# Kernel optimization log

Measured on AMD Instinct MI355X. Metric: run time of the kernel, lower is better.

## Reference

```python
import math
import jax, jax.numpy as jnp
import numpy as np

B, H, N, D = 1, 16, 4096, 64
SINK_SIZE = 32
NUM_PROJS = 7
BLOCK_SIZE = 256
SAMPLE_SIZE = 256
MIN_SEQ_LEN = 1024
_SAMPLE_KEY = jax.random.key(1234)

def _hamming_perm(num_projs):
    a = np.array([0, 1])
    for _ in range(num_projs - 1):
        a = np.concatenate([a, a[::-1] + a.shape[0]])
    return jnp.asarray(a, dtype=jnp.int32)

_PERM = _hamming_perm(NUM_PROJS)
_MASK = jnp.asarray(2 ** np.arange(NUM_PROJS), dtype=jnp.int32)

def lsh_hash(x, proj_dir):
    # x: [b,h,n,d], proj_dir: [d,r] -> Gray-code-permuted bucket ids [b,h,n]
    rotated = jnp.einsum('bhnd,dr->bhnr', x, proj_dir)
    bin_ids = jnp.sum((rotated > 0).astype(jnp.int32) * _MASK, axis=-1)
    return _PERM[bin_ids]

def indexing(x, idx, chunk_size=-1):
    # gather rows along axis 2, optionally zero-pad to a multiple of chunk_size
    out = jnp.take_along_axis(x, idx[..., None], axis=2)
    if chunk_size > 0 and out.shape[2] % chunk_size != 0:
        pad = (-out.shape[2]) % chunk_size
        out = jnp.pad(out, ((0, 0), (0, 0), (0, pad), (0, 0)))
    return out

def exact_attention(q, k, v, scale, causal=False, bias=None):
    qk = jnp.einsum('bhqd,bhkd->bhqk', q, k) * scale
    if causal:
        nq, nk = q.shape[2], k.shape[2]
        cmask = jnp.triu(jnp.full((nq, nk), jnp.finfo(q.dtype).min, dtype=q.dtype), k=1)
        qk = qk + cmask
    if bias is not None:
        qk = qk + bias
    lse = jax.nn.logsumexp(qk, axis=-1, keepdims=True)
    attn = jnp.einsum('bhqk,bhkd->bhqd', jnp.exp(qk - lse), v)
    return attn, lse

def add_self_attentions(attn1, lse1, attn2, lse2):
    # attn = (attn1*e^lse1 + attn2*e^lse2)/(e^lse1+e^lse2); lse = log(e^lse1+e^lse2)
    c = jax.nn.sigmoid(lse1 - lse2)
    attn = c * attn1 + (1 - c) * attn2
    lse = jnp.logaddexp(lse1, lse2)
    return attn, lse

def forward_no_causal_mask(q, k, v, scale, proj_dir, ctr):
    b, h, nq, d = q.shape
    nk = k.shape[2]
    if MIN_SEQ_LEN > nq:
        return exact_attention(q, k, v, scale, causal=False)
    # 1) sortLSH block-diagonal attention
    q_sort_idx = jnp.argsort(lsh_hash(q, proj_dir), axis=2)  # stable
    k_sort_idx = jnp.argsort(lsh_hash(k, proj_dir), axis=2)
    q_sort_idx_inv = jnp.argsort(q_sort_idx, axis=2)
    q_sorted = indexing(q, q_sort_idx, BLOCK_SIZE)
    k_sorted = indexing(k, k_sort_idx, BLOCK_SIZE)
    v_sorted = indexing(v, k_sort_idx, BLOCK_SIZE)
    num_blocks = k_sorted.shape[2] // BLOCK_SIZE
    q_block = q_sorted.shape[2] // num_blocks
    qs = q_sorted.reshape(-1, 1, q_block, d)
    ks = k_sorted.reshape(-1, 1, BLOCK_SIZE, d)
    vs = v_sorted.reshape(-1, 1, BLOCK_SIZE, d)
    attn_block, lse_block = exact_attention(qs, ks, vs, scale, causal=False)
    attn_block = attn_block.reshape(b, h, q_sorted.shape[2], d)[:, :, :nq, :]
    lse_block = lse_block.reshape(b, h, q_sorted.shape[2], 1)[:, :, :nq, :]
    q_sorted = q_sorted[:, :, :nq, :]
    k_sorted = k_sorted[:, :, :nk, :]
    v_sorted = v_sorted[:, :, :nk, :]
    # 2) residual via uniform sampling (block-diag entries masked out)
    if SAMPLE_SIZE > 0 and nq > q_block and nk > BLOCK_SIZE:
        skey = jax.random.fold_in(_SAMPLE_KEY, ctr[0]); ctr[0] += 1
        sampled = jax.random.randint(skey, (b, h, SAMPLE_SIZE), 0, nk)
        v_sub = indexing(v_sorted, sampled)
        k_sub = indexing(k_sorted, sampled)
        q_blk_id = jnp.arange(nq) // q_block                 # [nq]
        k_blk_id = sampled // BLOCK_SIZE                     # [b,h,s]
        bias = (q_blk_id[None, None, :, None] == k_blk_id[:, :, None, :]).astype(q.dtype) * jnp.finfo(q.dtype).min
        attn_res, lse_res = exact_attention(q_sorted, k_sub, v_sub, scale, causal=False, bias=bias)
        lse_res = lse_res + math.log(nk / SAMPLE_SIZE)
        attn, lse = add_self_attentions(attn_block, lse_block, attn_res, lse_res)
    else:
        attn, lse = attn_block, lse_block
    # restore original row order
    attn = indexing(attn, q_sort_idx_inv)
    lse = indexing(lse, q_sort_idx_inv)
    return attn, lse

def hyper_causal(q, k, v, scale, proj_dir, ctr):
    b, h, n, d = q.shape
    if n <= MIN_SEQ_LEN:
        return exact_attention(q, k, v, scale, causal=True)
    n_orig = n
    if n % 2:
        q = jnp.pad(q, ((0, 0), (0, 0), (0, 1), (0, 0)))
        k = jnp.pad(k, ((0, 0), (0, 0), (0, 1), (0, 0)))
        v = jnp.pad(v, ((0, 0), (0, 0), (0, 1), (0, 0)))
    half = q.shape[2] // 2
    # recurse on the two diagonal halves (folded into head dim)
    attn_bd, lse_bd = hyper_causal(q.reshape(b, 2 * h, half, d), k.reshape(b, 2 * h, half, d), v.reshape(b, 2 * h, half, d), scale, proj_dir, ctr)
    attn_bd = attn_bd.reshape(b, h, -1, d)
    lse_bd = lse_bd.reshape(b, h, -1, 1)
    # off-diagonal lower-left block, unmasked
    attn_un, lse_un = forward_no_causal_mask(q[:, :, half:, :], k[:, :, :half, :], v[:, :, :half, :], scale, proj_dir, ctr)
    attn_up, lse_up = attn_bd[:, :, :half, :], lse_bd[:, :, :half, :]
    attn_dn, lse_dn = add_self_attentions(attn_bd[:, :, half:, :], lse_bd[:, :, half:, :], attn_un, lse_un)
    attn = jnp.concatenate([attn_up, attn_dn], axis=2)
    lse = jnp.concatenate([lse_up, lse_dn], axis=2)
    if n_orig % 2:
        attn = attn[:, :, :-1, :]
        lse = lse[:, :, :-1, :]
    return attn, lse

def _forward(query, key, value, proj_dir):
    b, h, n, d = query.shape
    scale = d ** (-0.5)
    sink = min(SINK_SIZE, n)
    prefix_attn, prefix_lse = exact_attention(query, key[:, :, :sink, :], value[:, :, :sink, :], scale, causal=True)
    if sink >= n:
        return prefix_attn
    ctr = [0]
    tail_attn, tail_lse = hyper_causal(query[:, :, sink:, :], key[:, :, sink:, :], value[:, :, sink:, :], scale, proj_dir, ctr)
    padded_tail_attn = jnp.zeros_like(prefix_attn).at[:, :, sink:, :].set(tail_attn)
    neg_inf = jnp.full_like(prefix_lse[:, :, :sink, :], jnp.finfo(prefix_lse.dtype).min)
    padded_tail_lse = jnp.concatenate([neg_inf, tail_lse], axis=2)
    attn, _ = add_self_attentions(prefix_attn, prefix_lse, padded_tail_attn, padded_tail_lse)
    return attn

def setup_inputs() -> dict:
    rng = jax.random.key(0)
    k1, k2, k3, k4 = jax.random.split(rng, 4)
    return {
        'query': jax.random.normal(k1, (B, H, N, D), jnp.float32),
        'key': jax.random.normal(k2, (B, H, N, D), jnp.float32),
        'value': jax.random.normal(k3, (B, H, N, D), jnp.float32),
        'proj_dir': jax.random.normal(k4, (D, NUM_PROJS), jnp.float32),
    }

def reference(query, key, value, proj_dir):
    return _forward(query, key, value, proj_dir)
```

## Files before the change

kernel.cpp:

```cpp
#include <hip/hip_runtime.h>
#include <hip/hip_bf16.h>
#include <math.h>
#include <stdint.h>

#define H_ 16
#define N_ 4096
#define NT_ 4064
#define NL_ 2032
#define SINK_ 32
#define SAMP_ 256
#define SCALE_ 0.125f
#define QSCALE_ 0.18033688f
#define M0L2_ 11.5415606f
#define M0_ 8.0f
#define NEGBIG_ -3.0e38f
#define LOGOFF_L2_ 2.9886841f

typedef unsigned int uint;
typedef unsigned short ushort;
typedef short bf16x8 __attribute__((ext_vector_type(8)));
typedef float f32x4 __attribute__((ext_vector_type(4)));

union B8 { uint4 u; bf16x8 b; };

__device__ __forceinline__ f32x4 mfma16(const B8& a, const B8& b, f32x4 c) {
  return __builtin_amdgcn_mfma_f32_16x16x32_bf16(a.b, b.b, c, 0, 0, 0);
}

__device__ __forceinline__ uint bfpack(float a, float b) {
  uint ua = __float_as_uint(a), ub = __float_as_uint(b);
  ua += 0x7fffu + ((ua >> 16) & 1u);
  ub += 0x7fffu + ((ub >> 16) & 1u);
  return (ua >> 16) | (ub & 0xffff0000u);
}

__device__ __forceinline__ uint cvtpk(float a, float b) {
  union { __hip_bfloat162 h; uint u; } r;
  r.h.x = __float2bfloat16(a);
  r.h.y = __float2bfloat16(b);
  return r.u;
}

__device__ __forceinline__ float logaddexpf_(float a, float b) {
  float mx = fmaxf(a, b);
  return mx + __logf(__expf(a - mx) + __expf(b - mx));
}

__device__ __forceinline__ uint32_t rotl32_(uint32_t v, uint32_t d) {
  return (v << d) | (v >> (32u - d));
}

__device__ inline void tf2x32(uint32_t k0, uint32_t k1, uint32_t& x0, uint32_t& x1) {
  uint32_t ks2 = k0 ^ k1 ^ 0x1BD11BDAu;
  x0 += k0; x1 += k1;
#define TFR(r) { x0 += x1; x1 = rotl32_(x1, r); x1 ^= x0; }
  TFR(13u) TFR(15u) TFR(26u) TFR(6u)
  x0 += k1;  x1 += ks2 + 1u;
  TFR(17u) TFR(29u) TFR(16u) TFR(24u)
  x0 += ks2; x1 += k0 + 2u;
  TFR(13u) TFR(15u) TFR(26u) TFR(6u)
  x0 += k0;  x1 += k1 + 3u;
  TFR(17u) TFR(29u) TFR(16u) TFR(24u)
  x0 += k1;  x1 += ks2 + 4u;
  TFR(13u) TFR(15u) TFR(26u) TFR(6u)
  x0 += ks2; x1 += k0 + 5u;
#undef TFR
}

__device__ __forceinline__ void nomax_sm(f32x4 s[4], float& ssum) {
#pragma unroll
  for (int st = 0; st < 4; ++st)
#pragma unroll
    for (int r = 0; r < 4; ++r) {
      s[st][r] = __builtin_exp2f(s[st][r]);
      ssum += s[st][r];
    }
}

__device__ __forceinline__ void pv144(const f32x4 s[4], f32x4 o[4],
                                      const char* vbase, char* pw, int g) {
#pragma unroll
  for (int hk2 = 0; hk2 < 2; ++hk2) {
    const f32x4 pa = s[2 * hk2], pc = s[2 * hk2 + 1];
    *(uint2*)(pw + 8 * g)      = make_uint2(cvtpk(pa[0], pa[1]), cvtpk(pa[2], pa[3]));
    *(uint2*)(pw + 32 + 8 * g) = make_uint2(cvtpk(pc[0], pc[1]), cvtpk(pc[2], pc[3]));
    B8 pf, vf;
    pf.u = *(const uint4*)(pw + g * 16);
    vf.u = *(const uint4*)(vbase + 0 * 2304 + hk2 * 64); o[0] = mfma16(vf, pf, o[0]);
    vf.u = *(const uint4*)(vbase + 1 * 2304 + hk2 * 64); o[1] = mfma16(vf, pf, o[1]);
    vf.u = *(const uint4*)(vbase + 2 * 2304 + hk2 * 64); o[2] = mfma16(vf, pf, o[2]);
    vf.u = *(const uint4*)(vbase + 3 * 2304 + hk2 * 64); o[3] = mfma16(vf, pf, o[3]);
  }
}

__global__ __launch_bounds__(256) void kern_packhash(
    const float* __restrict__ K, const float* __restrict__ V, const float* __restrict__ Q,
    const float* __restrict__ proj,
    ushort* __restrict__ Kb, ushort* __restrict__ Vb, ushort* __restrict__ Vt,
    int* __restrict__ hq, int* __restrict__ hk) {
  const int bb = blockIdx.x;
  const int tid = threadIdx.x;
  if (bb < 2048) {
    const size_t idx = (size_t)bb * 256 + tid;
    const float4* s = (const float4*)(K + idx * 8);
    float4 f0 = s[0], f1 = s[1];
    uint4 p = make_uint4(bfpack(f0.x, f0.y), bfpack(f0.z, f0.w),
                         bfpack(f1.x, f1.y), bfpack(f1.z, f1.w));
    *(uint4*)(Kb + idx * 8) = p;
    return;
  }
  if (bb < 3072) {
    __shared__ ushort tr[64 * 72];
    const int u = bb - 2048;
    const int h = u >> 6, nt = u & 63;
    const int n0 = nt * 64;
    const size_t hN = (size_t)h * N_;
    const int nloc = tid >> 2, dpart = (tid & 3) * 16;
    const float4* src = (const float4*)(V + (hN + n0 + nloc) * 64 + dpart);
    float4 f0 = src[0], f1 = src[1], f2 = src[2], f3 = src[3];
    uint p0 = bfpack(f0.x, f0.y), p1 = bfpack(f0.z, f0.w);
    uint p2 = bfpack(f1.x, f1.y), p3 = bfpack(f1.z, f1.w);
    uint p4 = bfpack(f2.x, f2.y), p5 = bfpack(f2.z, f2.w);
    uint p6 = bfpack(f3.x, f3.y), p7 = bfpack(f3.z, f3.w);
    ushort* vbdst = Vb + (hN + n0 + nloc) * 64 + dpart;
    ((uint4*)vbdst)[0] = make_uint4(p0, p1, p2, p3);
    ((uint4*)vbdst)[1] = make_uint4(p4, p5, p6, p7);
    uint pv[8] = {p0, p1, p2, p3, p4, p5, p6, p7};
#pragma unroll
    for (int j = 0; j < 8; ++j) {
      tr[(dpart + 2 * j    ) * 72 + nloc] = (ushort)(pv[j] & 0xffffu);
      tr[(dpart + 2 * j + 1) * 72 + nloc] = (ushort)(pv[j] >> 16);
    }
    __syncthreads();
    const int d = tid >> 2, np = (tid & 3) * 16;
    const uint4* tp = (const uint4*)(tr + d * 72 + np);
    uint4 t0 = tp[0], t1 = tp[1];
    ushort* dst = Vt + ((size_t)(h * 64 + d)) * 4096 + n0 + np;
    ((uint4*)dst)[0] = t0;
    ((uint4*)dst)[1] = t1;
    return;
  }
  __shared__ float pr[448];
  const int u = bb - 3072;
  const int h = u & 15, tile = (u >> 4) & 7, which = u >> 7;
  for (int t = tid; t < 448; t += 256) pr[t] = proj[t];
  __syncthreads();
  const int i = tile * 256 + tid;
  if (i >= NL_) return;
  const int orig = (which == 0) ? (SINK_ + NL_ + i) : (SINK_ + i);
  const float4* x = (const float4*)((which == 0 ? Q : K) + ((size_t)h * N_ + orig) * 64);
  float xr[64];
#pragma unroll
  for (int d = 0; d < 16; ++d) {
    float4 g = x[d];
    xr[4*d+0] = g.x; xr[4*d+1] = g.y; xr[4*d+2] = g.z; xr[4*d+3] = g.w;
  }
  int bin = 0;
#pragma unroll
  for (int r = 0; r < 7; ++r) {
    float acc = 0.f;
#pragma unroll
    for (int d = 0; d < 64; ++d) acc = fmaf(xr[d], pr[d * 7 + r], acc);
    if (acc > 0.f) bin |= (1 << r);
  }
  const int g = bin ^ (bin >> 1);
  (which == 0 ? hq : hk)[h * NL_ + i] = g;
}

__global__ __launch_bounds__(256) void kern_sortsamp(
    const int* __restrict__ hq, const int* __restrict__ hk,
    int* __restrict__ q_sort, int* __restrict__ k_sort,
    int* __restrict__ samp_pos, int* __restrict__ samp_orig) {
  const int h = blockIdx.x, which = blockIdx.y;
  const int tid = threadIdx.x;

  __shared__ unsigned char keys8[NL_];
  __shared__ ushort M[64 * 130];
  __shared__ int btot[128];
  __shared__ int bscan[128];
  __shared__ ushort srt[NL_];

  const int* src = (which == 0 ? hq : hk) + h * NL_;
  for (int u = tid; u < 64 * 130 / 2; u += 256) ((uint*)M)[u] = 0u;
  for (int u = tid; u < NL_; u += 256) keys8[u] = (unsigned char)src[u];
  __syncthreads();

  if (tid < 64) {
    const int c = tid;
#pragma unroll 4
    for (int j = 0; j < 32; ++j) {
      const int u = c * 32 + j;
      if (u < NL_) ++M[c * 130 + keys8[u]];
    }
  }
  __syncthreads();

  if (tid < 128) {
    const int b = tid;
    int run = 0;
    for (int c = 0; c < 64; ++c) {
      const int v = M[c * 130 + b];
      M[c * 130 + b] = (ushort)run;
      run += v;
    }
    btot[b] = run;
    bscan[b] = run;
  }
  __syncthreads();

  for (int ofs = 1; ofs < 128; ofs <<= 1) {
    int v = 0;
    if (tid < 128 && tid >= ofs) v = bscan[tid - ofs];
    __syncthreads();
    if (tid < 128) bscan[tid] += v;
    __syncthreads();
  }

  int* dst = (which == 0 ? q_sort : k_sort) + h * NL_;
  if (tid < 64) {
    const int c = tid;
    for (int j = 0; j < 32; ++j) {
      const int u = c * 32 + j;
      if (u < NL_) {
        const int k = keys8[u];
        const int pos = (bscan[k] - btot[k]) + M[c * 130 + k];
        M[c * 130 + k] += 1;
        dst[pos] = u;
        srt[pos] = (ushort)u;
      }
    }
  }
  __syncthreads();

  if (which == 1) {
    const int s = tid;
    uint32_t a0 = 0u, a1 = 0u; tf2x32(0u, 1234u, a0, a1);
    uint32_t b0 = 0u, b1 = 0u; tf2x32(a0, a1, b0, b1);
    uint32_t c0 = 0u, c1 = 1u; tf2x32(a0, a1, c0, c1);
    const uint32_t j = (uint32_t)(h * SAMP_ + s);
    uint32_t h0 = 0u, h1 = j; tf2x32(b0, b1, h0, h1);
    uint32_t l0 = 0u, l1 = j; tf2x32(c0, c1, l0, l1);
    const uint32_t Hb = h0 ^ h1, Lb = l0 ^ l1;
    const uint32_t off = ((Hb % 2032u) * 16u + (Lb % 2032u)) % 2032u;
    samp_pos[h * SAMP_ + s] = (int)off;
    samp_orig[h * SAMP_ + s] = (int)srt[off];
  }
}

__global__ __launch_bounds__(256) void kern_attn_mfma(
    const float* __restrict__ Q, const ushort* __restrict__ Kb, const ushort* __restrict__ Vt,
    float* __restrict__ tail_attn, float* __restrict__ tail_lse,
    float* __restrict__ attn2, float* __restrict__ lse2) {
  __shared__ uint kk[4608];
  __shared__ uint vv[4352];
  __shared__ uint pbuf[1280];

  const int b = blockIdx.x;
  const int tid = threadIdx.x;
  const int lane = tid & 63, w = tid >> 6;
  const int g = lane >> 4, q = lane & 15;
  const uint4 z4 = make_uint4(0, 0, 0, 0);
  const f32x4 accb = {-M0L2_, -M0L2_, -M0L2_, -M0L2_};

  int h, q0, qbase, kbase, ntiles, p2vh = 0, chunkc = 0;
  bool causal;
  if (b < 256) {
    const int vh = b & 31; const int qt = b >> 5;
    h = vh >> 1; const int pp = vh & 1;
    q0 = qt * 128;
    qbase = SINK_ + pp * 2032 + 1016;
    kbase = SINK_ + pp * 2032;
    ntiles = 8; causal = false; p2vh = vh;
  } else {
    const int u = b - 256; const int vh = u & 63;
    const int qt = 7 - (u >> 6);
    h = vh >> 2; chunkc = vh & 3;
    q0 = qt * 128;
    qbase = SINK_ + chunkc * 1016;
    kbase = qbase;
    ntiles = qt + 1; causal = true;
  }
  const size_t hN = (size_t)h * N_;
  const int qrowA = q0 + w * 16 + q;
  const int qrowB = qrowA + 64;
  const int qcA = min(qrowA, 1015), qcB = min(qrowB, 1015);
  const int qwA_lo = q0 + w * 16, qwmaxA = qwA_lo + 15;
  const int qwB_lo = qwA_lo + 64;

  B8 qbA0, qbA1, qbB0, qbB1;
  {
    const float4* qp = (const float4*)(Q + (hN + qbase + qcA) * 64);
    float4 a = qp[2*g], c = qp[2*g+1], d = qp[8+2*g], e = qp[8+2*g+1];
    qbA0.u = make_uint4(bfpack(a.x*QSCALE_, a.y*QSCALE_), bfpack(a.z*QSCALE_, a.w*QSCALE_),
                        bfpack(c.x*QSCALE_, c.y*QSCALE_), bfpack(c.z*QSCALE_, c.w*QSCALE_));
    qbA1.u = make_uint4(bfpack(d.x*QSCALE_, d.y*QSCALE_), bfpack(d.z*QSCALE_, d.w*QSCALE_),
                        bfpack(e.x*QSCALE_, e.y*QSCALE_), bfpack(e.z*QSCALE_, e.w*QSCALE_));
    const float4* qp2 = (const float4*)(Q + (hN + qbase + qcB) * 64);
    a = qp2[2*g]; c = qp2[2*g+1]; d = qp2[8+2*g]; e = qp2[8+2*g+1];
    qbB0.u = make_uint4(bfpack(a.x*QSCALE_, a.y*QSCALE_), bfpack(a.z*QSCALE_, a.w*QSCALE_),
                        bfpack(c.x*QSCALE_, c.y*QSCALE_), bfpack(c.z*QSCALE_, c.w*QSCALE_));
    qbB1.u = make_uint4(bfpack(d.x*QSCALE_, d.y*QSCALE_), bfpack(d.z*QSCALE_, d.w*QSCALE_),
                        bfpack(e.x*QSCALE_, e.y*QSCALE_), bfpack(e.z*QSCALE_, e.w*QSCALE_));
  }
  f32x4 oA[4] = {{0,0,0,0},{0,0,0,0},{0,0,0,0},{0,0,0,0}};
  f32x4 oB[4] = {{0,0,0,0},{0,0,0,0},{0,0,0,0},{0,0,0,0}};
  float ssA = 0.f, ssB = 0.f;

  const int krow_l = tid >> 1, kpart = tid & 1;
  const int vrow = tid >> 2, vc32 = tid & 3;
  char* kdst = (char*)kk + krow_l * 144 + kpart * 64;
  char* vdst = (char*)vv + vrow * 272 + vc32 * 64;
  const char* kq = (const char*)kk + q * 144 + g * 16;
  const char* vq = (const char*)vv + q * 272 + g * 16;
  char* pw = (char*)pbuf + w * 1280 + q * 80;
  const size_t vtbase = ((size_t)(h * 64 + vrow)) * 4096 + kbase + vc32 * 32;

  uint4 kp0, kp1, kp2, kp3, va, va2, vb_, vb2;

#define LOADK(T) { const int kr = (T) * 128 + krow_l; \
    if (kr < 1016) { const uint4* s = (const uint4*)(Kb + (hN + kbase + kr) * 64 + kpart * 32); \
      kp0 = s[0]; kp1 = s[1]; kp2 = s[2]; kp3 = s[3]; } \
    else { kp0 = z4; kp1 = z4; kp2 = z4; kp3 = z4; } }
#define LOADV(T) { const uint4* sv = (const uint4*)(Vt + vtbase + (size_t)(T) * 128); \
    va = sv[0]; va2 = sv[1]; vb_ = sv[2]; vb2 = sv[3]; }

  LOADK(0) LOADV(0)

  for (int t = 0; t < ntiles; ++t) {
    const int kt = t * 128;
    __syncthreads();
    *(uint4*)kdst = kp0; *(uint4*)(kdst + 16) = kp1;
    *(uint4*)(kdst + 32) = kp2; *(uint4*)(kdst + 48) = kp3;
    *(uint4*)vdst = va; *(uint4*)(vdst + 16) = va2;
    *(uint4*)(vdst + 32) = vb_; *(uint4*)(vdst + 48) = vb2;
    __syncthreads();
    if (t + 1 < ntiles) { LOADK(t + 1) LOADV(t + 1) }

#pragma unroll
    for (int u2 = 0; u2 < 2; ++u2) {
      const int hb = kt + u2 * 64;
      const bool dA = !(causal && hb > qwmaxA);
      f32x4 sA[4], sB[4];
#pragma unroll
      for (int st = 0; st < 4; ++st) {
        B8 ka, kb2;
        ka.u  = *(const uint4*)(kq + (u2 * 64 + st * 16) * 144);
        kb2.u = *(const uint4*)(kq + (u2 * 64 + st * 16) * 144 + 64);
        if (dA) {
          f32x4 acc = accb;
          acc = mfma16(ka, qbA0, acc); acc = mfma16(kb2, qbA1, acc);
          sA[st] = acc;
        }
        f32x4 acc2 = accb;
        acc2 = mfma16(ka, qbB0, acc2); acc2 = mfma16(kb2, qbB1, acc2);
        sB[st] = acc2;
      }

      if (causal) {
        const int kb0 = hb + 4 * g;
        if (dA && hb + 63 > qwA_lo) {
#pragma unroll
          for (int st = 0; st < 4; ++st)
#pragma unroll
            for (int r = 0; r < 4; ++r)
              if (kb0 + st * 16 + r > qrowA) sA[st][r] = NEGBIG_;
        }
        if (hb + 63 > qwB_lo) {
#pragma unroll
          for (int st = 0; st < 4; ++st)
#pragma unroll
            for (int r = 0; r < 4; ++r)
              if (kb0 + st * 16 + r > qrowB) sB[st][r] = NEGBIG_;
        }
      } else if (hb + 63 >= 1016) {
        const int kb0 = hb + 4 * g;
#pragma unroll
        for (int st = 0; st < 4; ++st)
#pragma unroll
          for (int r = 0; r < 4; ++r)
            if (kb0 + st * 16 + r >= 1016) { sA[st][r] = NEGBIG_; sB[st][r] = NEGBIG_; }
      }

#define PVX(SS, OO) { \
      _Pragma("unroll") \
      for (int hk2 = 0; hk2 < 2; ++hk2) { \
        const f32x4 pa = SS[2 * hk2], pc = SS[2 * hk2 + 1]; \
        *(uint2*)(pw + 8 * g)      = make_uint2(cvtpk(pa[0], pa[1]), cvtpk(pa[2], pa[3])); \
        *(uint2*)(pw + 32 + 8 * g) = make_uint2(cvtpk(pc[0], pc[1]), cvtpk(pc[2], pc[3])); \
        B8 pf, vf; \
        pf.u = *(const uint4*)(pw + g * 16); \
        const int vo = u2 * 128 + hk2 * 64; \
        vf.u = *(const uint4*)(vq + 0 * 4352 + vo); OO[0] = mfma16(vf, pf, OO[0]); \
        vf.u = *(const uint4*)(vq + 1 * 4352 + vo); OO[1] = mfma16(vf, pf, OO[1]); \
        vf.u = *(const uint4*)(vq + 2 * 4352 + vo); OO[2] = mfma16(vf, pf, OO[2]); \
        vf.u = *(const uint4*)(vq + 3 * 4352 + vo); OO[3] = mfma16(vf, pf, OO[3]); \
      } }

      if (dA) {
        nomax_sm(sA, ssA);
        PVX(sA, oA)
      }
      nomax_sm(sB, ssB);
      PVX(sB, oB)
#undef PVX
    }
  }
#undef LOADK
#undef LOADV

  ssA += __shfl_xor(ssA, 16); ssA += __shfl_xor(ssA, 32);
  ssB += __shfl_xor(ssB, 16); ssB += __shfl_xor(ssB, 32);
#pragma unroll
  for (int fr = 0; fr < 2; ++fr) {
    const int qrow = fr == 0 ? qrowA : qrowB;
    if (qrow >= 1016) continue;
    f32x4* o = fr == 0 ? oA : oB;
    const float ss = fr == 0 ? ssA : ssB;
    const float lse = M0_ + __logf(ss);
    const float inv = 1.f / ss;
    if (causal) {
      const int trow = chunkc * 1016 + qrow;
      float* tp = tail_attn + ((size_t)h * NT_ + trow) * 64;
      *(f32x4*)(tp +  0 + 4*g) = o[0] * inv;
      *(f32x4*)(tp + 16 + 4*g) = o[1] * inv;
      *(f32x4*)(tp + 32 + 4*g) = o[2] * inv;
      *(f32x4*)(tp + 48 + 4*g) = o[3] * inv;
      if (lane < 16) tail_lse[h * NT_ + trow] = lse;
    } else {
      float* tp = attn2 + ((size_t)p2vh * 1016 + qrow) * 64;
      *(f32x4*)(tp +  0 + 4*g) = o[0] * inv;
      *(f32x4*)(tp + 16 + 4*g) = o[1] * inv;
      *(f32x4*)(tp + 32 + 4*g) = o[2] * inv;
      *(f32x4*)(tp + 48 + 4*g) = o[3] * inv;
      if (lane < 16) lse2[p2vh * 1016 + qrow] = lse;
    }
  }
}

__global__ __launch_bounds__(256) void kern_lsh_mfma(
    const float* __restrict__ Q, const ushort* __restrict__ Kb, const ushort* __restrict__ Vb,
    const int* __restrict__ q_sort, const int* __restrict__ k_sort,
    const int* __restrict__ samp_pos, const int* __restrict__ samp_orig,
    float* __restrict__ attn3, float* __restrict__ lse3) {
  __shared__ uint kk[2304];
  __shared__ uint vv[2304];
  __shared__ uint pbuf[1280];
  __shared__ float bias_s[64];

  const int b = blockIdx.x;
  const int h = b >> 4, pt = b & 15;
  const int tid = threadIdx.x;
  const int lane = tid & 63, w = tid >> 6;
  const int g = lane >> 4, q = lane & 15;
  const int blkq = pt >> 1;
  const size_t hN = (size_t)h * N_;

  const int pA = pt * 128 + w * 16 + q;
  const int pB = pA + 64;
  const int qiA = q_sort[h * NL_ + min(pA, NL_ - 1)];
  const int qiB = q_sort[h * NL_ + min(pB, NL_ - 1)];

  const int skey = tid >> 2, kpart = tid & 3;
  const int kpi = tid & 31, vdb = (tid >> 5) * 8;
  int kidx[8], vi0[8], vi1[8];
#pragma unroll
  for (int t = 0; t < 8; ++t) {
    if (t < 4) {
      const int slot = blkq * 256 + t * 64 + skey;
      kidx[t] = (slot < NL_) ? k_sort[h * NL_ + slot] : -1;
      const int s0 = blkq * 256 + t * 64 + 2 * kpi;
      vi0[t] = (s0 < NL_) ? k_sort[h * NL_ + s0] : -1;
      vi1[t] = (s0 + 1 < NL_) ? k_sort[h * NL_ + s0 + 1] : -1;
    } else {
      kidx[t] = samp_orig[h * SAMP_ + (t - 4) * 64 + skey];
      const int si = (t - 4) * 64 + 2 * kpi;
      vi0[t] = samp_orig[h * SAMP_ + si];
      vi1[t] = samp_orig[h * SAMP_ + si + 1];
    }
  }
  float biasr[4];
  if (tid < 64) {
#pragma unroll
    for (int j = 0; j < 4; ++j)
      biasr[j] = ((samp_pos[h * SAMP_ + j * 64 + tid] >> 8) == blkq) ? NEGBIG_ : LOGOFF_L2_;
  }

  B8 qbA0, qbA1, qbB0, qbB1;
  {
    const float4* qp = (const float4*)(Q + (hN + SINK_ + NL_ + qiA) * 64);
    float4 a = qp[2*g], c = qp[2*g+1], d = qp[8+2*g], e = qp[8+2*g+1];
    qbA0.u = make_uint4(bfpack(a.x*QSCALE_, a.y*QSCALE_), bfpack(a.z*QSCALE_, a.w*QSCALE_),
                        bfpack(c.x*QSCALE_, c.y*QSCALE_), bfpack(c.z*QSCALE_, c.w*QSCALE_));
    qbA1.u = make_uint4(bfpack(d.x*QSCALE_, d.y*QSCALE_), bfpack(d.z*QSCALE_, d.w*QSCALE_),
                        bfpack(e.x*QSCALE_, e.y*QSCALE_), bfpack(e.z*QSCALE_, e.w*QSCALE_));
    const float4* qp2 = (const float4*)(Q + (hN + SINK_ + NL_ + qiB) * 64);
    a = qp2[2*g]; c = qp2[2*g+1]; d = qp2[8+2*g]; e = qp2[8+2*g+1];
    qbB0.u = make_uint4(bfpack(a.x*QSCALE_, a.y*QSCALE_), bfpack(a.z*QSCALE_, a.w*QSCALE_),
                        bfpack(c.x*QSCALE_, c.y*QSCALE_), bfpack(c.z*QSCALE_, c.w*QSCALE_));
    qbB1.u = make_uint4(bfpack(d.x*QSCALE_, d.y*QSCALE_), bfpack(d.z*QSCALE_, d.w*QSCALE_),
                        bfpack(e.x*QSCALE_, e.y*QSCALE_), bfpack(e.z*QSCALE_, e.w*QSCALE_));
  }
  f32x4 oA[4] = {{0,0,0,0},{0,0,0,0},{0,0,0,0},{0,0,0,0}};
  f32x4 oB[4] = {{0,0,0,0},{0,0,0,0},{0,0,0,0},{0,0,0,0}};
  float ssA = 0.f, ssB = 0.f;
  const f32x4 accb = {-M0L2_, -M0L2_, -M0L2_, -M0L2_};

  char* kdst = (char*)kk + skey * 144 + kpart * 32;
  char* vdst = (char*)vv + vdb * 144 + kpi * 4;
  const char* kq = (const char*)kk + q * 144 + g * 16;
  const char* vq = (const char*)vv + q * 144 + g * 16;
  char* pw = (char*)pbuf + w * 1280 + q * 80;

  const uint4 z4 = make_uint4(0, 0, 0, 0);
  uint4 kp0, kp1, va, vb_;

#define LLOADK(T) { const int kr = kidx[T]; \
    if (kr >= 0) { const uint4* s = (const uint4*)(Kb + (hN + SINK_ + kr) * 64 + kpart * 16); \
      kp0 = s[0]; kp1 = s[1]; } else { kp0 = z4; kp1 = z4; } }
#define LLOADV(T) { const int r0 = vi0[T], r1 = vi1[T]; \
    va  = (r0 >= 0) ? *(const uint4*)(Vb + (hN + SINK_ + r0) * 64 + vdb) : z4; \
    vb_ = (r1 >= 0) ? *(const uint4*)(Vb + (hN + SINK_ + r1) * 64 + vdb) : z4; }

  LLOADK(0) LLOADV(0)

  for (int t = 0; t < 8; ++t) {
    __syncthreads();
    *(uint4*)kdst = kp0; *(uint4*)(kdst + 16) = kp1;
#define VP(JW, AW, BW) { \
    *(uint*)(vdst + (2*(JW)) * 144) = (AW & 0xffffu) | (BW << 16); \
    *(uint*)(vdst + (2*(JW) + 1) * 144) = (AW >> 16) | (BW & 0xffff0000u); }
    VP(0, va.x, vb_.x) VP(1, va.y, vb_.y) VP(2, va.z, vb_.z) VP(3, va.w, vb_.w)
#undef VP
    if (t >= 4 && tid < 64) bias_s[tid] = biasr[t - 4];
    __syncthreads();
    if (t + 1 < 8) { LLOADK(t + 1) LLOADV(t + 1) }

    f32x4 sA[4], sB[4];
#pragma unroll
    for (int st = 0; st < 4; ++st) {
      B8 ka, kb2;
      ka.u  = *(const uint4*)(kq + (st * 16) * 144);
      kb2.u = *(const uint4*)(kq + (st * 16) * 144 + 64);
      f32x4 acc = accb;
      acc = mfma16(ka, qbA0, acc); acc = mfma16(kb2, qbA1, acc);
      sA[st] = acc;
      f32x4 acc2 = accb;
      acc2 = mfma16(ka, qbB0, acc2); acc2 = mfma16(kb2, qbB1, acc2);
      sB[st] = acc2;
    }
    if (t >= 4) {
      const f32x4* bp = (const f32x4*)bias_s;
#pragma unroll
      for (int st = 0; st < 4; ++st) {
        sA[st] = sA[st] + bp[st * 4 + g];
        sB[st] = sB[st] + bp[st * 4 + g];
      }
    }

    nomax_sm(sA, ssA);
    pv144(sA, oA, vq, pw, g);
    nomax_sm(sB, ssB);
    pv144(sB, oB, vq, pw, g);
  }
#undef LLOADK
#undef LLOADV

  ssA += __shfl_xor(ssA, 16); ssA += __shfl_xor(ssA, 32);
  ssB += __shfl_xor(ssB, 16); ssB += __shfl_xor(ssB, 32);
#pragma unroll
  for (int fr = 0; fr < 2; ++fr) {
    const int p = fr == 0 ? pA : pB;
    if (p >= NL_) continue;
    const int qi = fr == 0 ? qiA : qiB;
    f32x4* o = fr == 0 ? oA : oB;
    const float ss = fr == 0 ? ssA : ssB;
    const float un = M0_ + __logf(ss);
    const float inv = 1.f / ss;
    float* tp = attn3 + ((size_t)h * NL_ + qi) * 64;
    *(f32x4*)(tp +  0 + 4*g) = o[0] * inv;
    *(f32x4*)(tp + 16 + 4*g) = o[1] * inv;
    *(f32x4*)(tp + 32 + 4*g) = o[2] * inv;
    *(f32x4*)(tp + 48 + 4*g) = o[3] * inv;
    if (lane < 16) lse3[h * NL_ + qi] = un;
  }
}

__global__ __launch_bounds__(256) void kern_final(
    const float* __restrict__ Q, const float* __restrict__ K, const float* __restrict__ V,
    const float* __restrict__ tail_attn, const float* __restrict__ tail_lse,
    const float* __restrict__ attn2, const float* __restrict__ lse2,
    const float* __restrict__ attn3, const float* __restrict__ lse3,
    float* __restrict__ out) {
  const int h = blockIdx.x;
  const int r = blockIdx.y * 256 + (int)threadIdx.x;

  __shared__ float4 kk[SINK_ * 16];
  __shared__ float4 vv[SINK_ * 16];
  for (int u = threadIdx.x; u < SINK_ * 16; u += 256) {
    const int row = u >> 4, d4 = u & 15;
    kk[u] = ((const float4*)(K + ((size_t)h * N_ + row) * 64))[d4];
    vv[u] = ((const float4*)(V + ((size_t)h * N_ + row) * 64))[d4];
  }
  __syncthreads();

  float4 q4[16], acc[16];
  const float4* qp = (const float4*)(Q + ((size_t)h * N_ + r) * 64);
#pragma unroll
  for (int d = 0; d < 16; ++d) { q4[d] = qp[d]; acc[d] = make_float4(0.f, 0.f, 0.f, 0.f); }

  float m = -INFINITY, ssum = 0.f;
  const int nk = min(SINK_, r + 1);
  for (int j = 0; j < nk; ++j) {
    float s = 0.f;
#pragma unroll
    for (int d = 0; d < 16; ++d) {
      float4 x = q4[d], y = kk[j * 16 + d];
      s = fmaf(x.x, y.x, s); s = fmaf(x.y, y.y, s);
      s = fmaf(x.z, y.z, s); s = fmaf(x.w, y.w, s);
    }
    s *= SCALE_;
    const float nm = fmaxf(m, s);
    const float f = __expf(m - nm), wgt = __expf(s - nm);
    ssum = ssum * f + wgt;
    const float4* v4 = &vv[j * 16];
#pragma unroll
    for (int d = 0; d < 16; ++d) {
      acc[d].x = acc[d].x * f + wgt * v4[d].x;
      acc[d].y = acc[d].y * f + wgt * v4[d].y;
      acc[d].z = acc[d].z * f + wgt * v4[d].z;
      acc[d].w = acc[d].w * f + wgt * v4[d].w;
    }
    m = nm;
  }
  const float pl = m + __logf(ssum);
  const float inv = 1.f / ssum;
  float4* op = (float4*)(out + ((size_t)h * N_ + r) * 64);
  if (r < SINK_) {
#pragma unroll
    for (int d = 0; d < 16; ++d)
      op[d] = make_float4(acc[d].x * inv, acc[d].y * inv, acc[d].z * inv, acc[d].w * inv);
    return;
  }

  const int t = r - SINK_;
  float4 a[16];
  const float4* tp = (const float4*)(tail_attn + ((size_t)h * NT_ + t) * 64);
#pragma unroll
  for (int d = 0; d < 16; ++d) a[d] = tp[d];
  float al = tail_lse[h * NT_ + t];

  const int pp = (t >= NL_) ? 1 : 0;
  const int tloc = t - pp * NL_;
  if (tloc >= 1016) {
    const int vh = h * 2 + pp, i = tloc - 1016;
    const float l2 = lse2[vh * 1016 + i];
    const float c = 1.f / (1.f + __expf(l2 - al));
    const float4* bp = (const float4*)(attn2 + ((size_t)vh * 1016 + i) * 64);
#pragma unroll
    for (int d = 0; d < 16; ++d) {
      const float4 bb = bp[d];
      a[d] = make_float4(c * a[d].x + (1.f - c) * bb.x,
                         c * a[d].y + (1.f - c) * bb.y,
                         c * a[d].z + (1.f - c) * bb.z,
                         c * a[d].w + (1.f - c) * bb.w);
    }
    al = logaddexpf_(al, l2);
  }
  if (t >= NL_) {
    const int qi = t - NL_;
    const float l3 = lse3[h * NL_ + qi];
    const float c = 1.f / (1.f + __expf(l3 - al));
    const float4* bp = (const float4*)(attn3 + ((size_t)h * NL_ + qi) * 64);
#pragma unroll
    for (int d = 0; d < 16; ++d) {
      const float4 bb = bp[d];
      a[d] = make_float4(c * a[d].x + (1.f - c) * bb.x,
                         c * a[d].y + (1.f - c) * bb.y,
                         c * a[d].z + (1.f - c) * bb.z,
                         c * a[d].w + (1.f - c) * bb.w);
    }
    al = logaddexpf_(al, l3);
  }
  const float cc = 1.f / (1.f + __expf(al - pl));
#pragma unroll
  for (int d = 0; d < 16; ++d)
    op[d] = make_float4(cc * acc[d].x * inv + (1.f - cc) * a[d].x,
                        cc * acc[d].y * inv + (1.f - cc) * a[d].y,
                        cc * acc[d].z * inv + (1.f - cc) * a[d].z,
                        cc * acc[d].w * inv + (1.f - cc) * a[d].w);
}

extern "C" void kernel_launch(void* const* d_in, const int* in_sizes, int n_in,
                              void* d_out, int out_size, void* d_ws, size_t ws_size,
                              hipStream_t stream) {
  (void)in_sizes; (void)n_in; (void)out_size; (void)ws_size;
  const float* Q = (const float*)d_in[0];
  const float* K = (const float*)d_in[1];
  const float* V = (const float*)d_in[2];
  const float* proj = (const float*)d_in[3];
  float* out = (float*)d_out;

  char* w = (char*)d_ws;
  auto carve = [&](size_t bytes) { char* p = w; w += (bytes + 255) & ~(size_t)255; return p; };
  float* tail_attn = (float*)carve((size_t)H_ * NT_ * 64 * sizeof(float));
  float* tail_lse  = (float*)carve((size_t)H_ * NT_ * sizeof(float));
  float* attn2     = (float*)carve((size_t)32 * 1016 * 64 * sizeof(float));
  float* lse2      = (float*)carve((size_t)32 * 1016 * sizeof(float));
  float* attn3     = (float*)carve((size_t)H_ * NL_ * 64 * sizeof(float));
  float* lse3      = (float*)carve((size_t)H_ * NL_ * sizeof(float));
  ushort* Kb     = (ushort*)carve((size_t)H_ * N_ * 64 * sizeof(ushort));
  ushort* Vb     = (ushort*)carve((size_t)H_ * N_ * 64 * sizeof(ushort));
  ushort* Vt     = (ushort*)carve((size_t)H_ * N_ * 64 * sizeof(ushort) + 4096);
  int* hq        = (int*)carve((size_t)H_ * NL_ * sizeof(int));
  int* hk        = (int*)carve((size_t)H_ * NL_ * sizeof(int));
  int* q_sort    = (int*)carve((size_t)H_ * NL_ * sizeof(int));
  int* k_sort    = (int*)carve((size_t)H_ * NL_ * sizeof(int));
  int* samp_pos  = (int*)carve((size_t)H_ * SAMP_ * sizeof(int));
  int* samp_orig = (int*)carve((size_t)H_ * SAMP_ * sizeof(int));

  kern_packhash<<<dim3(3328), 256, 0, stream>>>(K, V, Q, proj, Kb, Vb, Vt, hq, hk);
  kern_sortsamp<<<dim3(H_, 2), 256, 0, stream>>>(hq, hk, q_sort, k_sort, samp_pos, samp_orig);
  kern_attn_mfma<<<dim3(768), 256, 0, stream>>>(Q, Kb, Vt, tail_attn, tail_lse, attn2, lse2);
  kern_lsh_mfma<<<dim3(256), 256, 0, stream>>>(Q, Kb, Vb, q_sort, k_sort, samp_pos, samp_orig,
                                               attn3, lse3);
  kern_final<<<dim3(H_, 16), 256, 0, stream>>>(Q, K, V, tail_attn, tail_lse,
                                               attn2, lse2, attn3, lse3, out);
}
```

Measured before the change: 149.4 us.

## Split key ranges across more blocks and merge partial results in final kernel

```diff
diff --git a/kernel.cpp b/kernel.cpp
--- a/kernel.cpp
+++ b/kernel.cpp
@@ -79,6 +79,7 @@
 
 __device__ __forceinline__ void pv144(const f32x4 s[4], f32x4 o[4],
                                       const char* vbase, char* pw, int g) {
+  __builtin_amdgcn_s_setprio(1);
 #pragma unroll
   for (int hk2 = 0; hk2 < 2; ++hk2) {
     const f32x4 pa = s[2 * hk2], pc = s[2 * hk2 + 1];
@@ -91,6 +92,7 @@
     vf.u = *(const uint4*)(vbase + 2 * 2304 + hk2 * 64); o[2] = mfma16(vf, pf, o[2]);
     vf.u = *(const uint4*)(vbase + 3 * 2304 + hk2 * 64); o[3] = mfma16(vf, pf, o[3]);
   }
+  __builtin_amdgcn_s_setprio(0);
 }
 
 __global__ __launch_bounds__(256) void kern_packhash(
@@ -262,23 +264,25 @@
   const uint4 z4 = make_uint4(0, 0, 0, 0);
   const f32x4 accb = {-M0L2_, -M0L2_, -M0L2_, -M0L2_};
 
-  int h, q0, qbase, kbase, ntiles, p2vh = 0, chunkc = 0;
+  int h, q0, qbase, kbase, ntiles, klen, p2slot = 0, chunkc = 0;
   bool causal;
-  if (b < 256) {
-    const int vh = b & 31; const int qt = b >> 5;
-    h = vh >> 1; const int pp = vh & 1;
-    q0 = qt * 128;
-    qbase = SINK_ + pp * 2032 + 1016;
-    kbase = SINK_ + pp * 2032;
-    ntiles = 8; causal = false; p2vh = vh;
-  } else {
-    const int u = b - 256; const int vh = u & 63;
+  if (b < 512) {
+    const int u = b; const int vh = u & 63;
     const int qt = 7 - (u >> 6);
     h = vh >> 2; chunkc = vh & 3;
     q0 = qt * 128;
     qbase = SINK_ + chunkc * 1016;
     kbase = qbase;
-    ntiles = qt + 1; causal = true;
+    ntiles = qt + 1; causal = true; klen = 1016;
+  } else {
+    const int u = b - 512; const int vh = u & 31; const int qt = (u >> 5) & 7;
+    const int hf = u >> 8;
+    h = vh >> 1; const int pp = vh & 1;
+    q0 = qt * 128;
+    qbase = SINK_ + pp * 2032 + 1016;
+    kbase = SINK_ + pp * 2032 + hf * 512;
+    ntiles = 4; causal = false; klen = hf ? 504 : 512;
+    p2slot = hf * 32 * 1016 + vh * 1016;
   }
   const size_t hN = (size_t)h * N_;
   const int qrowA = q0 + w * 16 + q;
@@ -318,7 +322,7 @@
   uint4 kp0, kp1, kp2, kp3, va, va2, vb_, vb2;
 
 #define LOADK(T) { const int kr = (T) * 128 + krow_l; \
-    if (kr < 1016) { const uint4* s = (const uint4*)(Kb + (hN + kbase + kr) * 64 + kpart * 32); \
+    if (kr < klen) { const uint4* s = (const uint4*)(Kb + (hN + kbase + kr) * 64 + kpart * 32); \
       kp0 = s[0]; kp1 = s[1]; kp2 = s[2]; kp3 = s[3]; } \
     else { kp0 = z4; kp1 = z4; kp2 = z4; kp3 = z4; } }
 #define LOADV(T) { const uint4* sv = (const uint4*)(Vt + vtbase + (size_t)(T) * 128); \
@@ -341,6 +345,7 @@
       const int hb = kt + u2 * 64;
       const bool dA = !(causal && hb > qwmaxA);
       f32x4 sA[4], sB[4];
+      __builtin_amdgcn_s_setprio(1);
 #pragma unroll
       for (int st = 0; st < 4; ++st) {
         B8 ka, kb2;
@@ -355,6 +360,7 @@
         acc2 = mfma16(ka, qbB0, acc2); acc2 = mfma16(kb2, qbB1, acc2);
         sB[st] = acc2;
       }
+      __builtin_amdgcn_s_setprio(0);
 
       if (causal) {
         const int kb0 = hb + 4 * g;
@@ -372,16 +378,17 @@
             for (int r = 0; r < 4; ++r)
               if (kb0 + st * 16 + r > qrowB) sB[st][r] = NEGBIG_;
         }
-      } else if (hb + 63 >= 1016) {
+      } else if (hb + 63 >= klen) {
         const int kb0 = hb + 4 * g;
 #pragma unroll
         for (int st = 0; st < 4; ++st)
 #pragma unroll
           for (int r = 0; r < 4; ++r)
-            if (kb0 + st * 16 + r >= 1016) { sA[st][r] = NEGBIG_; sB[st][r] = NEGBIG_; }
+            if (kb0 + st * 16 + r >= klen) { sA[st][r] = NEGBIG_; sB[st][r] = NEGBIG_; }
       }
 
 #define PVX(SS, OO) { \
+      __builtin_amdgcn_s_setprio(1); \
       _Pragma("unroll") \
       for (int hk2 = 0; hk2 < 2; ++hk2) { \
         const f32x4 pa = SS[2 * hk2], pc = SS[2 * hk2 + 1]; \
@@ -394,7 +401,8 @@
         vf.u = *(const uint4*)(vq + 1 * 4352 + vo); OO[1] = mfma16(vf, pf, OO[1]); \
         vf.u = *(const uint4*)(vq + 2 * 4352 + vo); OO[2] = mfma16(vf, pf, OO[2]); \
         vf.u = *(const uint4*)(vq + 3 * 4352 + vo); OO[3] = mfma16(vf, pf, OO[3]); \
-      } }
+      } \
+      __builtin_amdgcn_s_setprio(0); }
 
       if (dA) {
         nomax_sm(sA, ssA);
@@ -427,12 +435,12 @@
       *(f32x4*)(tp + 48 + 4*g) = o[3] * inv;
       if (lane < 16) tail_lse[h * NT_ + trow] = lse;
     } else {
-      float* tp = attn2 + ((size_t)p2vh * 1016 + qrow) * 64;
+      float* tp = attn2 + ((size_t)(p2slot + qrow)) * 64;
       *(f32x4*)(tp +  0 + 4*g) = o[0] * inv;
       *(f32x4*)(tp + 16 + 4*g) = o[1] * inv;
       *(f32x4*)(tp + 32 + 4*g) = o[2] * inv;
       *(f32x4*)(tp + 48 + 4*g) = o[3] * inv;
-      if (lane < 16) lse2[p2vh * 1016 + qrow] = lse;
+      if (lane < 16) lse2[p2slot + qrow] = lse;
     }
   }
 }
@@ -448,7 +456,9 @@
   __shared__ float bias_s[64];
 
   const int b = blockIdx.x;
-  const int h = b >> 4, pt = b & 15;
+  const int which = b >> 8;
+  const int bq = b & 255;
+  const int h = bq >> 4, pt = bq & 15;
   const int tid = threadIdx.x;
   const int lane = tid & 63, w = tid >> 6;
   const int g = lane >> 4, q = lane & 15;
@@ -462,24 +472,24 @@
 
   const int skey = tid >> 2, kpart = tid & 3;
   const int kpi = tid & 31, vdb = (tid >> 5) * 8;
-  int kidx[8], vi0[8], vi1[8];
-#pragma unroll
-  for (int t = 0; t < 8; ++t) {
-    if (t < 4) {
+  int kidx[4], vi0[4], vi1[4];
+  float biasr[4];
+#pragma unroll
+  for (int t = 0; t < 4; ++t) {
+    if (which == 0) {
       const int slot = blkq * 256 + t * 64 + skey;
       kidx[t] = (slot < NL_) ? k_sort[h * NL_ + slot] : -1;
       const int s0 = blkq * 256 + t * 64 + 2 * kpi;
       vi0[t] = (s0 < NL_) ? k_sort[h * NL_ + s0] : -1;
       vi1[t] = (s0 + 1 < NL_) ? k_sort[h * NL_ + s0 + 1] : -1;
     } else {
-      kidx[t] = samp_orig[h * SAMP_ + (t - 4) * 64 + skey];
-      const int si = (t - 4) * 64 + 2 * kpi;
+      kidx[t] = samp_orig[h * SAMP_ + t * 64 + skey];
+      const int si = t * 64 + 2 * kpi;
       vi0[t] = samp_orig[h * SAMP_ + si];
       vi1[t] = samp_orig[h * SAMP_ + si + 1];
     }
   }
-  float biasr[4];
-  if (tid < 64) {
+  if (which == 1 && tid < 64) {
 #pragma unroll
     for (int j = 0; j < 4; ++j)
       biasr[j] = ((samp_pos[h * SAMP_ + j * 64 + tid] >> 8) == blkq) ? NEGBIG_ : LOGOFF_L2_;
@@ -523,7 +533,7 @@
 
   LLOADK(0) LLOADV(0)
 
-  for (int t = 0; t < 8; ++t) {
+  for (int t = 0; t < 4; ++t) {
     __syncthreads();
     *(uint4*)kdst = kp0; *(uint4*)(kdst + 16) = kp1;
 #define VP(JW, AW, BW) { \
@@ -531,11 +541,12 @@
     *(uint*)(vdst + (2*(JW) + 1) * 144) = (AW >> 16) | (BW & 0xffff0000u); }
     VP(0, va.x, vb_.x) VP(1, va.y, vb_.y) VP(2, va.z, vb_.z) VP(3, va.w, vb_.w)
 #undef VP
-    if (t >= 4 && tid < 64) bias_s[tid] = biasr[t - 4];
+    if (which == 1 && tid < 64) bias_s[tid] = biasr[t];
     __syncthreads();
-    if (t + 1 < 8) { LLOADK(t + 1) LLOADV(t + 1) }
+    if (t + 1 < 4) { LLOADK(t + 1) LLOADV(t + 1) }
 
     f32x4 sA[4], sB[4];
+    __builtin_amdgcn_s_setprio(1);
 #pragma unroll
     for (int st = 0; st < 4; ++st) {
       B8 ka, kb2;
@@ -548,7 +559,8 @@
       acc2 = mfma16(ka, qbB0, acc2); acc2 = mfma16(kb2, qbB1, acc2);
       sB[st] = acc2;
     }
-    if (t >= 4) {
+    __builtin_amdgcn_s_setprio(0);
+    if (which == 1) {
       const f32x4* bp = (const f32x4*)bias_s;
 #pragma unroll
       for (int st = 0; st < 4; ++st) {
@@ -567,6 +579,7 @@
 
   ssA += __shfl_xor(ssA, 16); ssA += __shfl_xor(ssA, 32);
   ssB += __shfl_xor(ssB, 16); ssB += __shfl_xor(ssB, 32);
+  const size_t obase = (size_t)which * 16 * NL_;
 #pragma unroll
   for (int fr = 0; fr < 2; ++fr) {
     const int p = fr == 0 ? pA : pB;
@@ -576,12 +589,12 @@
     const float ss = fr == 0 ? ssA : ssB;
     const float un = M0_ + __logf(ss);
     const float inv = 1.f / ss;
-    float* tp = attn3 + ((size_t)h * NL_ + qi) * 64;
+    float* tp = attn3 + (obase + (size_t)h * NL_ + qi) * 64;
     *(f32x4*)(tp +  0 + 4*g) = o[0] * inv;
     *(f32x4*)(tp + 16 + 4*g) = o[1] * inv;
     *(f32x4*)(tp + 32 + 4*g) = o[2] * inv;
     *(f32x4*)(tp + 48 + 4*g) = o[3] * inv;
-    if (lane < 16) lse3[h * NL_ + qi] = un;
+    if (lane < 16) lse3[obase + h * NL_ + qi] = un;
   }
 }
 
@@ -608,7 +621,7 @@
 #pragma unroll
   for (int d = 0; d < 16; ++d) { q4[d] = qp[d]; acc[d] = make_float4(0.f, 0.f, 0.f, 0.f); }
 
-  float m = -INFINITY, ssum = 0.f;
+  float ssum = 0.f;
   const int nk = min(SINK_, r + 1);
   for (int j = 0; j < nk; ++j) {
     float s = 0.f;
@@ -618,21 +631,18 @@
       s = fmaf(x.x, y.x, s); s = fmaf(x.y, y.y, s);
       s = fmaf(x.z, y.z, s); s = fmaf(x.w, y.w, s);
     }
-    s *= SCALE_;
-    const float nm = fmaxf(m, s);
-    const float f = __expf(m - nm), wgt = __expf(s - nm);
-    ssum = ssum * f + wgt;
+    const float wgt = __expf(fmaf(s, SCALE_, -M0_));
+    ssum += wgt;
     const float4* v4 = &vv[j * 16];
 #pragma unroll
     for (int d = 0; d < 16; ++d) {
-      acc[d].x = acc[d].x * f + wgt * v4[d].x;
-      acc[d].y = acc[d].y * f + wgt * v4[d].y;
-      acc[d].z = acc[d].z * f + wgt * v4[d].z;
-      acc[d].w = acc[d].w * f + wgt * v4[d].w;
-    }
-    m = nm;
-  }
-  const float pl = m + __logf(ssum);
+      acc[d].x = fmaf(wgt, v4[d].x, acc[d].x);
+      acc[d].y = fmaf(wgt, v4[d].y, acc[d].y);
+      acc[d].z = fmaf(wgt, v4[d].z, acc[d].z);
+      acc[d].w = fmaf(wgt, v4[d].w, acc[d].w);
+    }
+  }
+  const float pl = M0_ + __logf(ssum);
   const float inv = 1.f / ssum;
   float4* op = (float4*)(out + ((size_t)h * N_ + r) * 64);
   if (r < SINK_) {
@@ -653,12 +663,20 @@
   const int tloc = t - pp * NL_;
   if (tloc >= 1016) {
     const int vh = h * 2 + pp, i = tloc - 1016;
-    const float l2 = lse2[vh * 1016 + i];
+    const float l20 = lse2[vh * 1016 + i];
+    const float l21 = lse2[32 * 1016 + vh * 1016 + i];
+    const float c12 = 1.f / (1.f + __expf(l21 - l20));
+    const float l2 = logaddexpf_(l20, l21);
     const float c = 1.f / (1.f + __expf(l2 - al));
-    const float4* bp = (const float4*)(attn2 + ((size_t)vh * 1016 + i) * 64);
+    const float4* b0 = (const float4*)(attn2 + ((size_t)(vh * 1016 + i)) * 64);
+    const float4* b1 = (const float4*)(attn2 + ((size_t)(32 * 1016 + vh * 1016 + i)) * 64);
 #pragma unroll
     for (int d = 0; d < 16; ++d) {
-      const float4 bb = bp[d];
+      const float4 x0 = b0[d], x1 = b1[d];
+      const float4 bb = make_float4(c12 * x0.x + (1.f - c12) * x1.x,
+                                    c12 * x0.y + (1.f - c12) * x1.y,
+                                    c12 * x0.z + (1.f - c12) * x1.z,
+                                    c12 * x0.w + (1.f - c12) * x1.w);
       a[d] = make_float4(c * a[d].x + (1.f - c) * bb.x,
                          c * a[d].y + (1.f - c) * bb.y,
                          c * a[d].z + (1.f - c) * bb.z,
@@ -668,12 +686,20 @@
   }
   if (t >= NL_) {
     const int qi = t - NL_;
-    const float l3 = lse3[h * NL_ + qi];
+    const float l3a = lse3[h * NL_ + qi];
+    const float l3b = lse3[16 * NL_ + h * NL_ + qi];
+    const float c34 = 1.f / (1.f + __expf(l3b - l3a));
+    const float l3 = logaddexpf_(l3a, l3b);
     const float c = 1.f / (1.f + __expf(l3 - al));
-    const float4* bp = (const float4*)(attn3 + ((size_t)h * NL_ + qi) * 64);
+    const float4* b0 = (const float4*)(attn3 + ((size_t)(h * NL_ + qi)) * 64);
+    const float4* b1 = (const float4*)(attn3 + ((size_t)(16 * NL_ + h * NL_ + qi)) * 64);
 #pragma unroll
     for (int d = 0; d < 16; ++d) {
-      const float4 bb = bp[d];
+      const float4 x0 = b0[d], x1 = b1[d];
+      const float4 bb = make_float4(c34 * x0.x + (1.f - c34) * x1.x,
+                                    c34 * x0.y + (1.f - c34) * x1.y,
+                                    c34 * x0.z + (1.f - c34) * x1.z,
+                                    c34 * x0.w + (1.f - c34) * x1.w);
       a[d] = make_float4(c * a[d].x + (1.f - c) * bb.x,
                          c * a[d].y + (1.f - c) * bb.y,
                          c * a[d].z + (1.f - c) * bb.z,
@@ -704,10 +730,10 @@
   auto carve = [&](size_t bytes) { char* p = w; w += (bytes + 255) & ~(size_t)255; return p; };
   float* tail_attn = (float*)carve((size_t)H_ * NT_ * 64 * sizeof(float));
   float* tail_lse  = (float*)carve((size_t)H_ * NT_ * sizeof(float));
-  float* attn2     = (float*)carve((size_t)32 * 1016 * 64 * sizeof(float));
-  float* lse2      = (float*)carve((size_t)32 * 1016 * sizeof(float));
-  float* attn3     = (float*)carve((size_t)H_ * NL_ * 64 * sizeof(float));
-  float* lse3      = (float*)carve((size_t)H_ * NL_ * sizeof(float));
+  float* attn2     = (float*)carve((size_t)2 * 32 * 1016 * 64 * sizeof(float));
+  float* lse2      = (float*)carve((size_t)2 * 32 * 1016 * sizeof(float));
+  float* attn3     = (float*)carve((size_t)2 * H_ * NL_ * 64 * sizeof(float));
+  float* lse3      = (float*)carve((size_t)2 * H_ * NL_ * sizeof(float));
   ushort* Kb     = (ushort*)carve((size_t)H_ * N_ * 64 * sizeof(ushort));
   ushort* Vb     = (ushort*)carve((size_t)H_ * N_ * 64 * sizeof(ushort));
   ushort* Vt     = (ushort*)carve((size_t)H_ * N_ * 64 * sizeof(ushort) + 4096);
@@ -720,8 +746,8 @@
 
   kern_packhash<<<dim3(3328), 256, 0, stream>>>(K, V, Q, proj, Kb, Vb, Vt, hq, hk);
   kern_sortsamp<<<dim3(H_, 2), 256, 0, stream>>>(hq, hk, q_sort, k_sort, samp_pos, samp_orig);
-  kern_attn_mfma<<<dim3(768), 256, 0, stream>>>(Q, Kb, Vt, tail_attn, tail_lse, attn2, lse2);
-  kern_lsh_mfma<<<dim3(256), 256, 0, stream>>>(Q, Kb, Vb, q_sort, k_sort, samp_pos, samp_orig,
+  kern_attn_mfma<<<dim3(1024), 256, 0, stream>>>(Q, Kb, Vt, tail_attn, tail_lse, attn2, lse2);
+  kern_lsh_mfma<<<dim3(512), 256, 0, stream>>>(Q, Kb, Vb, q_sort, k_sort, samp_pos, samp_orig,
                                                attn3, lse3);
   kern_final<<<dim3(H_, 16), 256, 0, stream>>>(Q, K, V, tail_attn, tail_lse,
                                                attn2, lse2, attn3, lse3, out);
```

Measured after the change: 134.0 us. -10.4%, faster.
